# Performance work log

Hardware: AMD Instinct MI355X
Metric: run time of the kernel (lower is better)

## Reference

```python
import jax, jax.numpy as jnp
import numpy as np

DIM = 2048
N_HEADS = 32
N_KV_HEADS = 8
HEAD_DIM = DIM // N_HEADS  # 64
N_REP = N_HEADS // N_KV_HEADS  # 4
BSZ = 2
SEQ = 2048


def setup_inputs() -> dict:
    key = jax.random.key(0)
    ks = jax.random.split(key, 7)
    s = 0.02
    return {
        "x": jax.random.normal(ks[0], (BSZ, SEQ, DIM), dtype=jnp.float32),
        "freqs_cos": jnp.cos(jnp.outer(jnp.arange(SEQ, dtype=jnp.float32),
                                       1.0 / (10000.0 ** (jnp.arange(0, HEAD_DIM, 2, dtype=jnp.float32) / HEAD_DIM)))),
        "freqs_sin": jnp.sin(jnp.outer(jnp.arange(SEQ, dtype=jnp.float32),
                                       1.0 / (10000.0 ** (jnp.arange(0, HEAD_DIM, 2, dtype=jnp.float32) / HEAD_DIM)))),
        "wq": jax.random.normal(ks[1], (DIM, N_HEADS * HEAD_DIM), dtype=jnp.float32) * s,
        "wk": jax.random.normal(ks[2], (DIM, N_KV_HEADS * HEAD_DIM), dtype=jnp.float32) * s,
        "wv": jax.random.normal(ks[3], (DIM, N_KV_HEADS * HEAD_DIM), dtype=jnp.float32) * s,
        "wo": jax.random.normal(ks[4], (N_HEADS * HEAD_DIM, DIM), dtype=jnp.float32) * s,
    }


def _apply_rope(t, cos, sin):
    # t: [b, s, h, hd]; cos/sin: [s, hd/2] -> broadcast [1, s, 1, hd/2]
    tr = t.reshape(t.shape[:-1] + (HEAD_DIM // 2, 2))
    t_r, t_i = tr[..., 0], tr[..., 1]
    c = cos[None, :, None, :]
    s = sin[None, :, None, :]
    out_r = t_r * c - t_i * s
    out_i = t_r * s + t_i * c
    return jnp.stack([out_r, out_i], axis=-1).reshape(t.shape)


def reference(x, freqs_cos, freqs_sin, wq, wk, wv, wo):
    b, s, _ = x.shape
    xq = (x @ wq).reshape(b, s, N_HEADS, HEAD_DIM)
    xk = (x @ wk).reshape(b, s, N_KV_HEADS, HEAD_DIM)
    xv = (x @ wv).reshape(b, s, N_KV_HEADS, HEAD_DIM)

    xq = _apply_rope(xq, freqs_cos, freqs_sin)
    xk = _apply_rope(xk, freqs_cos, freqs_sin)

    # GQA: group query heads over kv heads instead of materializing repeated KV
    # xq -> [b, kv_heads, n_rep, s, hd]
    q = xq.transpose(0, 2, 1, 3).reshape(b, N_KV_HEADS, N_REP, s, HEAD_DIM)
    k = xk.transpose(0, 2, 1, 3)  # [b, kv, s, hd]
    v = xv.transpose(0, 2, 1, 3)  # [b, kv, s, hd]

    scale = 1.0 / jnp.sqrt(jnp.asarray(HEAD_DIM, dtype=x.dtype))
    scores = jnp.einsum("bgrqd,bgkd->bgrqk", q, k) * scale  # [b,kv,rep,s,s]
    causal = jnp.tril(jnp.ones((s, s), dtype=bool))
    scores = jnp.where(causal[None, None, None], scores, jnp.finfo(scores.dtype).min)
    probs = jax.nn.softmax(scores, axis=-1)
    out = jnp.einsum("bgrqk,bgkd->bgrqd", probs, v)  # [b,kv,rep,s,hd]
    out = out.reshape(b, N_HEADS, s, HEAD_DIM).transpose(0, 2, 1, 3).reshape(b, s, N_HEADS * HEAD_DIM)
    return out @ wo
```

## Files before the change

kernel.cpp:

```cpp
#include <hip/hip_runtime.h>

typedef unsigned short u16;
typedef unsigned int u32;
typedef __bf16 bf16x4 __attribute__((ext_vector_type(4)));
typedef __bf16 bf16x8 __attribute__((ext_vector_type(8)));
typedef float f32x4 __attribute__((ext_vector_type(4)));
typedef u32 u32x4 __attribute__((ext_vector_type(4)));

struct __align__(4) U16x2 { u16 x, y; };
struct __align__(8) U16x4 { u16 x, y, z, w; };

#define DEV static __device__ __forceinline__

extern "C" __device__ float __ocml_exp2_f32(float);
#if __has_builtin(__builtin_amdgcn_exp2f)
#define EXP2(x) __builtin_amdgcn_exp2f(x)
#else
#define EXP2(x) __ocml_exp2_f32(x)
#endif

DEV u16 f2bf(float f) {
  __bf16 h = (__bf16)f;
  return __builtin_bit_cast(u16, h);
}
DEV float bf2f(u16 u) { return __uint_as_float(((u32)u) << 16); }
DEV u32 pk2bf(float lo, float hi) { return (u32)f2bf(lo) | ((u32)f2bf(hi) << 16); }

DEV void gload16(const void* g, void* l) {
  __builtin_amdgcn_global_load_lds((const __attribute__((address_space(1))) char*)g,
                                   (__attribute__((address_space(3))) char*)l, 16, 0, 0);
}

DEV f32x4 mfma16(bf16x8 a, bf16x8 b, f32x4 c) {
  return __builtin_amdgcn_mfma_f32_16x16x32_bf16(a, b, c, 0, 0, 0);
}

__global__ __launch_bounds__(256) void cvt_x(const float* __restrict__ x, u16* __restrict__ xb) {
  int i = blockIdx.x * 256 + threadIdx.x;
  float4 v = ((const float4*)x)[i];
  U16x4 o;
  o.x = f2bf(v.x); o.y = f2bf(v.y); o.z = f2bf(v.z); o.w = f2bf(v.w);
  ((U16x4*)xb)[i] = o;
}

__global__ __launch_bounds__(256) void tconv(const float* __restrict__ src, u16* __restrict__ dst,
                                             int C, int nOff, int ldd) {
  __shared__ float t[32][33];
  int bx = blockIdx.x, by = blockIdx.y;
  int tx = threadIdx.x, ty = threadIdx.y;
#pragma unroll
  for (int j = 0; j < 4; ++j)
    t[ty + 8 * j][tx] = src[(size_t)(by * 32 + ty + 8 * j) * C + bx * 32 + tx];
  __syncthreads();
#pragma unroll
  for (int j = 0; j < 4; ++j)
    dst[(size_t)(nOff + bx * 32 + ty + 8 * j) * ldd + by * 32 + tx] = f2bf(t[tx][ty + 8 * j]);
}

__global__ __launch_bounds__(256) void vtrans(const u16* __restrict__ qkv, u16* __restrict__ Vt) {
  __shared__ u16 t[32][33];
  int bx = blockIdx.x, by = blockIdx.y, bz = blockIdx.z;
  int tx = threadIdx.x, ty = threadIdx.y;
  int b = bz >> 3, kh = bz & 7;
  const u16* src = qkv + (size_t)(b * 2048 + bx * 32) * 3072 + 2560 + kh * 64 + by * 32;
#pragma unroll
  for (int j = 0; j < 4; ++j) t[ty + 8 * j][tx] = src[(size_t)(ty + 8 * j) * 3072 + tx];
  __syncthreads();
  u16* dst = Vt + ((size_t)bz * 64 + by * 32) * 2048 + bx * 32;
#pragma unroll
  for (int j = 0; j < 4; ++j) dst[(size_t)(ty + 8 * j) * 2048 + tx] = t[tx][ty + 8 * j];
}

__global__ __launch_bounds__(256) void rope_qk(const u16* __restrict__ qkv,
                                               const float* __restrict__ fc,
                                               const float* __restrict__ fs,
                                               u16* __restrict__ Qo, u16* __restrict__ Ko) {
  int t = blockIdx.x * 256 + threadIdx.x;
  int d2 = t & 31;
  int rest = t >> 5;
  int h40 = rest % 40;
  int bs = rest / 40;
  int s = bs & 2047;
  int b = bs >> 11;
  const u16* src;
  u16* dst;
  float qscale;
  if (h40 < 32) {
    src = qkv + (size_t)bs * 3072 + h40 * 64 + 2 * d2;
    dst = Qo + (((size_t)(b * 32 + h40) * 2048 + s) * 64 + 2 * d2);
    qscale = 0.18033688011112042f;
  } else {
    int kh = h40 - 32;
    src = qkv + (size_t)bs * 3072 + 2048 + kh * 64 + 2 * d2;
    dst = Ko + (((size_t)(b * 8 + kh) * 2048 + s) * 64 + 2 * d2);
    qscale = 1.0f;
  }
  U16x2 v = *(const U16x2*)src;
  float xr = bf2f(v.x), xi = bf2f(v.y);
  float c = fc[s * 32 + d2] * qscale, sn = fs[s * 32 + d2] * qscale;
  U16x2 o;
  o.x = f2bf(xr * c - xi * sn);
  o.y = f2bf(xr * sn + xi * c);
  *(U16x2*)dst = o;
}

template <typename OutT>
__global__ __launch_bounds__(256, 2) void gemm_bt(const u16* __restrict__ A,
                                                  const u16* __restrict__ BT,
                                                  OutT* __restrict__ C,
                                                  int M, int N, int K) {
  __shared__ __align__(16) char smem[65536];
  const int tid = threadIdx.x;
  const int lane = tid & 63;
  const int wm = (tid >> 7) & 1, wn = (tid >> 6) & 1;
  const int tm = blockIdx.y, tn = blockIdx.x;
  const int Kb = K * 2;

  f32x4 acc[4][4];
#pragma unroll
  for (int i = 0; i < 4; ++i)
#pragma unroll
    for (int j = 0; j < 4; ++j) acc[i][j] = (f32x4){0.f, 0.f, 0.f, 0.f};

  const char* Ag = (const char*)A + (size_t)tm * 128 * Kb;
  const char* Bg = (const char*)BT + (size_t)tn * 128 * Kb;

  auto stage = [&](int buf, int t) {
#pragma unroll
    for (int i = 0; i < 4; ++i) {
      int vt = i * 256 + tid;
      int row = vt >> 3;
      int cb = (((vt & 7) << 4) ^ ((row & 7) << 4));
      gload16(Ag + (size_t)row * Kb + t * 128 + cb, smem + buf * 16384 + vt * 16);
      gload16(Bg + (size_t)row * Kb + t * 128 + cb, smem + 32768 + buf * 16384 + vt * 16);
    }
  };

  stage(0, 0);
  int cur = 0;
  const int NT = K >> 6;
  for (int t = 0; t < NT; ++t) {
    __syncthreads();
    if (t + 1 < NT) stage(cur ^ 1, t + 1);
    const char* As = smem + cur * 16384;
    const char* Bs = smem + 32768 + cur * 16384;
#pragma unroll
    for (int ks = 0; ks < 2; ++ks) {
      bf16x8 a[4], b[4];
#pragma unroll
      for (int mf = 0; mf < 4; ++mf) {
        int row = wm * 64 + mf * 16 + (lane & 15);
        int cb = (ks * 64 + ((lane >> 4) << 4)) ^ ((row & 7) << 4);
        a[mf] = *(const bf16x8*)(As + row * 128 + cb);
      }
#pragma unroll
      for (int nf = 0; nf < 4; ++nf) {
        int row = wn * 64 + nf * 16 + (lane & 15);
        int cb = (ks * 64 + ((lane >> 4) << 4)) ^ ((row & 7) << 4);
        b[nf] = *(const bf16x8*)(Bs + row * 128 + cb);
      }
#pragma unroll
      for (int mf = 0; mf < 4; ++mf)
#pragma unroll
        for (int nf = 0; nf < 4; ++nf) acc[mf][nf] = mfma16(a[mf], b[nf], acc[mf][nf]);
    }
    cur ^= 1;
  }
#pragma unroll
  for (int mf = 0; mf < 4; ++mf) {
    int row0 = tm * 128 + wm * 64 + mf * 16 + ((lane >> 4) << 2);
#pragma unroll
    for (int nf = 0; nf < 4; ++nf) {
      int col = tn * 128 + wn * 64 + nf * 16 + (lane & 15);
#pragma unroll
      for (int r = 0; r < 4; ++r) {
        float v = acc[mf][nf][r];
        if constexpr (sizeof(OutT) == 4)
          C[(size_t)(row0 + r) * N + col] = v;
        else
          C[(size_t)(row0 + r) * N + col] = f2bf(v);
      }
    }
  }
}

__global__ __launch_bounds__(128, 4) void attn(const u16* __restrict__ Q,
                                               const u16* __restrict__ Kt,
                                               const u16* __restrict__ Vt,
                                               u16* __restrict__ O) {
  __shared__ __align__(16) char smem[16384];

  const int tid = threadIdx.x, lane = tid & 63, w = tid >> 6;
  const int q15 = lane & 15, g = lane >> 4;
  const int bx = blockIdx.x, h = blockIdx.y, b = blockIdx.z;
  const int kh = h >> 2;
  const int QT0 = 63 - bx, QT1 = bx;

  const char* Qg = (const char*)(Q + ((size_t)(b * 32 + h) * 2048) * 64);
  const char* Kg = (const char*)(Kt + ((size_t)(b * 8 + kh) * 2048 * 64));
  const char* Vg = (const char*)(Vt + ((size_t)(b * 8 + kh) * 64 * 2048));

  bf16x8 qf0[2], qf1[2];
#pragma unroll
  for (int ks = 0; ks < 2; ++ks) {
    int r0 = QT0 * 32 + w * 16 + q15;
    int r1 = QT1 * 32 + w * 16 + q15;
    qf0[ks] = *(const bf16x8*)(Qg + (size_t)r0 * 128 + ks * 64 + (g << 4));
    qf1[ks] = *(const bf16x8*)(Qg + (size_t)r1 * 128 + ks * 64 + (g << 4));
  }

  f32x4 acc0[4], acc1[4];
#pragma unroll
  for (int j = 0; j < 4; ++j) {
    acc0[j] = (f32x4){0.f, 0.f, 0.f, 0.f};
    acc1[j] = (f32x4){0.f, 0.f, 0.f, 0.f};
  }
  float m0 = -1e30f, m1 = -1e30f, l0 = 0.f, l1 = 0.f;
  const f32x4 FZ = (f32x4){0.f, 0.f, 0.f, 0.f};

  auto stageKV = [&](int buf, int kt) {
#pragma unroll
    for (int i = 0; i < 2; ++i) {
      int vt = i * 128 + tid;
      int rho = vt >> 3, ck = vt & 7;
      int kap = ((rho & 12) << 1) + ((rho & 16) >> 2) + (rho & 3);
      gload16(Kg + (size_t)(kt * 32 + kap) * 128 + (((ck ^ rho) & 7) << 4),
              smem + buf * 8192 + vt * 16);
      int d = vt >> 2, cv = vt & 3;
      gload16(Vg + (size_t)d * 4096 + kt * 64 + (((cv ^ (d >> 1)) & 3) << 4),
              smem + buf * 8192 + 4096 + vt * 16);
    }
  };

  stageKV(0, 0);
  int cur = 0;
  const int nkt = QT0 + 1;
  for (int kt = 0; kt < nkt; ++kt) {
    __syncthreads();
    if (kt + 1 < nkt) stageKV(cur ^ 1, kt + 1);
    const char* Ks = smem + cur * 8192;
    const char* Vs = smem + cur * 8192 + 4096;
    const bool la = (kt <= QT1);

    bf16x8 kf[2][2];
#pragma unroll
    for (int ks = 0; ks < 2; ++ks)
#pragma unroll
      for (int nf = 0; nf < 2; ++nf) {
        int r = nf * 16 + q15;
        int c = (4 * ks + g) ^ (r & 7);
        kf[ks][nf] = *(const bf16x8*)(Ks + r * 128 + (c << 4));
      }

    f32x4 st0[2], st1[2];
    __builtin_amdgcn_s_setprio(1);
#pragma unroll
    for (int nf = 0; nf < 2; ++nf) {
      st0[nf] = mfma16(kf[0][nf], qf0[0], FZ);
      st0[nf] = mfma16(kf[1][nf], qf0[1], st0[nf]);
    }
    if (la) {
#pragma unroll
      for (int nf = 0; nf < 2; ++nf) {
        st1[nf] = mfma16(kf[0][nf], qf1[0], FZ);
        st1[nf] = mfma16(kf[1][nf], qf1[1], st1[nf]);
      }
    }
    __builtin_amdgcn_s_setprio(0);

    if (kt == QT0) {
      int qg = QT0 * 32 + w * 16 + q15;
#pragma unroll
      for (int nf = 0; nf < 2; ++nf)
#pragma unroll
        for (int r = 0; r < 4; ++r) {
          int kg = kt * 32 + 8 * g + 4 * nf + r;
          if (kg > qg) st0[nf][r] = -1e30f;
        }
    }
    if (la && kt == QT1) {
      int qg = QT1 * 32 + w * 16 + q15;
#pragma unroll
      for (int nf = 0; nf < 2; ++nf)
#pragma unroll
        for (int r = 0; r < 4; ++r) {
          int kg = kt * 32 + 8 * g + 4 * nf + r;
          if (kg > qg) st1[nf][r] = -1e30f;
        }
    }

    bf16x8 pa0, pa1;
#pragma unroll
    for (int t = 0; t < 2; ++t) {
      if (t == 1 && !la) break;
      f32x4* st = (t == 0) ? st0 : st1;
      float& m_r = (t == 0) ? m0 : m1;
      float& l_r = (t == 0) ? l0 : l1;
      f32x4* accT = (t == 0) ? acc0 : acc1;

      float vm = fmaxf(fmaxf(fmaxf(st[0][0], st[0][1]), fmaxf(st[0][2], st[0][3])),
                       fmaxf(fmaxf(st[1][0], st[1][1]), fmaxf(st[1][2], st[1][3])));
      vm = fmaxf(vm, __shfl_xor(vm, 16, 64));
      vm = fmaxf(vm, __shfl_xor(vm, 32, 64));
      const bool resc = !__all(vm - m_r <= 8.0f);
      if (resc) {
        float mn = fmaxf(m_r, vm);
        float cr = EXP2(m_r - mn);
        m_r = mn;
        l_r *= cr;
        float cra[4];
#pragma unroll
        for (int r = 0; r < 4; ++r) cra[r] = __shfl(cr, 4 * g + r, 64);
#pragma unroll
        for (int nfd = 0; nfd < 4; ++nfd)
#pragma unroll
          for (int r = 0; r < 4; ++r) accT[nfd][r] *= cra[r];
      }
      float vs = 0.f;
      u32x4 W;
      {
        float p0 = EXP2(st[0][0] - m_r), p1 = EXP2(st[0][1] - m_r);
        float p2 = EXP2(st[0][2] - m_r), p3 = EXP2(st[0][3] - m_r);
        float p4 = EXP2(st[1][0] - m_r), p5 = EXP2(st[1][1] - m_r);
        float p6 = EXP2(st[1][2] - m_r), p7 = EXP2(st[1][3] - m_r);
        vs = ((p0 + p1) + (p2 + p3)) + ((p4 + p5) + (p6 + p7));
        W.x = pk2bf(p0, p1);
        W.y = pk2bf(p2, p3);
        W.z = pk2bf(p4, p5);
        W.w = pk2bf(p6, p7);
      }
      if (t == 0) pa0 = __builtin_bit_cast(bf16x8, W);
      else pa1 = __builtin_bit_cast(bf16x8, W);
      vs += __shfl_xor(vs, 16, 64);
      vs += __shfl_xor(vs, 32, 64);
      l_r += vs;
    }

#pragma unroll
    for (int nfd = 0; nfd < 4; ++nfd) {
      int d = nfd * 16 + q15;
      int c = (g ^ (d >> 1)) & 3;
      bf16x8 vb = *(const bf16x8*)(Vs + d * 64 + (c << 4));
      __builtin_amdgcn_s_setprio(1);
      acc0[nfd] = mfma16(pa0, vb, acc0[nfd]);
      if (la) acc1[nfd] = mfma16(pa1, vb, acc1[nfd]);
      __builtin_amdgcn_s_setprio(0);
    }
    cur ^= 1;
  }

#pragma unroll
  for (int t = 0; t < 2; ++t) {
    float l_r = (t == 0) ? l0 : l1;
    f32x4* accT = (t == 0) ? acc0 : acc1;
    int qt = (t == 0) ? QT0 : QT1;
    u16* Og = O + ((size_t)(b * 2048 + qt * 32 + w * 16) * 2048 + h * 64);
    float la4[4];
#pragma unroll
    for (int r = 0; r < 4; ++r) la4[r] = __shfl(l_r, 4 * g + r, 64);
#pragma unroll
    for (int r = 0; r < 4; ++r) {
      float li = 1.f / la4[r];
#pragma unroll
      for (int nfd = 0; nfd < 4; ++nfd)
        Og[(size_t)(4 * g + r) * 2048 + nfd * 16 + q15] = f2bf(accT[nfd][r] * li);
    }
  }
}

extern "C" void kernel_launch(void* const* d_in, const int* in_sizes, int n_in,
                              void* d_out, int out_size, void* d_ws, size_t ws_size,
                              hipStream_t stream) {
  const float* x = (const float*)d_in[0];
  const float* fc = (const float*)d_in[1];
  const float* fs = (const float*)d_in[2];
  const float* wq = (const float*)d_in[3];
  const float* wk = (const float*)d_in[4];
  const float* wv = (const float*)d_in[5];
  const float* wo = (const float*)d_in[6];
  float* out = (float*)d_out;
  char* ws = (char*)d_ws;

  u16* xb    = (u16*)(ws);
  u16* qkv   = (u16*)(ws + 16777216);
  u16* woT   = (u16*)(ws + 41943040);
  u16* wqkvT = (u16*)(ws + 50331648);
  u16* Kbuf  = (u16*)(ws + 50331648);
  u16* Vtb   = (u16*)(ws + 54525952);
  u16* Qbuf = xb;
  u16* Obuf = qkv;

  dim3 tb(32, 8);
  cvt_x<<<dim3(8192), dim3(256), 0, stream>>>(x, xb);
  tconv<<<dim3(64, 64), tb, 0, stream>>>(wq, wqkvT, 2048, 0, 2048);
  tconv<<<dim3(16, 64), tb, 0, stream>>>(wk, wqkvT, 512, 2048, 2048);
  tconv<<<dim3(16, 64), tb, 0, stream>>>(wv, wqkvT, 512, 2560, 2048);
  tconv<<<dim3(64, 64), tb, 0, stream>>>(wo, woT, 2048, 0, 2048);
  gemm_bt<u16><<<dim3(24, 32), dim3(256), 0, stream>>>(xb, wqkvT, qkv, 4096, 3072, 2048);
  rope_qk<<<dim3(20480), dim3(256), 0, stream>>>(qkv, fc, fs, Qbuf, Kbuf);
  vtrans<<<dim3(64, 2, 16), tb, 0, stream>>>(qkv, Vtb);
  attn<<<dim3(32, 32, 2), dim3(128), 0, stream>>>(Qbuf, Kbuf, Vtb, Obuf);
  gemm_bt<float><<<dim3(16, 32), dim3(256), 0, stream>>>(Obuf, woT, out, 4096, 2048, 2048);
}
```

Before: 219.5 us.

## Fuse RoPE into QKV GEMM epilogue and restructure attention to 64-row query blocks

Applies RoPE and the query scale directly in the QKV GEMM epilogue, writing Q and K in head-major layout and V as a separate slice. This removes the rope_qk kernel and its extra pass over the qkv buffer. The attention kernel also changes from paired 32-row query tiles (balanced as 63-bx and bx) to a single 64-row block per 256-thread workgroup with 64-key tiles and a doubled LDS footprint. That drops the causal load-balancing pairing and the launch now runs longest blocks first. The epilogue also adds per-element shuffles and scattered frequency loads.

```diff
diff --git a/kernel.cpp b/kernel.cpp
--- a/kernel.cpp
+++ b/kernel.cpp
@@ -23,7 +23,6 @@
   __bf16 h = (__bf16)f;
   return __builtin_bit_cast(u16, h);
 }
-DEV float bf2f(u16 u) { return __uint_as_float(((u32)u) << 16); }
 DEV u32 pk2bf(float lo, float hi) { return (u32)f2bf(lo) | ((u32)f2bf(hi) << 16); }
 
 DEV void gload16(const void* g, void* l) {
@@ -57,64 +56,33 @@
     dst[(size_t)(nOff + bx * 32 + ty + 8 * j) * ldd + by * 32 + tx] = f2bf(t[tx][ty + 8 * j]);
 }
 
-__global__ __launch_bounds__(256) void vtrans(const u16* __restrict__ qkv, u16* __restrict__ Vt) {
+__global__ __launch_bounds__(256) void vtrans(const u16* __restrict__ Vsl, u16* __restrict__ Vt) {
   __shared__ u16 t[32][33];
   int bx = blockIdx.x, by = blockIdx.y, bz = blockIdx.z;
   int tx = threadIdx.x, ty = threadIdx.y;
   int b = bz >> 3, kh = bz & 7;
-  const u16* src = qkv + (size_t)(b * 2048 + bx * 32) * 3072 + 2560 + kh * 64 + by * 32;
-#pragma unroll
-  for (int j = 0; j < 4; ++j) t[ty + 8 * j][tx] = src[(size_t)(ty + 8 * j) * 3072 + tx];
+  const u16* src = Vsl + (size_t)(b * 2048 + bx * 32) * 512 + kh * 64 + by * 32;
+#pragma unroll
+  for (int j = 0; j < 4; ++j) t[ty + 8 * j][tx] = src[(size_t)(ty + 8 * j) * 512 + tx];
   __syncthreads();
   u16* dst = Vt + ((size_t)bz * 64 + by * 32) * 2048 + bx * 32;
 #pragma unroll
   for (int j = 0; j < 4; ++j) dst[(size_t)(ty + 8 * j) * 2048 + tx] = t[tx][ty + 8 * j];
 }
 
-__global__ __launch_bounds__(256) void rope_qk(const u16* __restrict__ qkv,
-                                               const float* __restrict__ fc,
-                                               const float* __restrict__ fs,
-                                               u16* __restrict__ Qo, u16* __restrict__ Ko) {
-  int t = blockIdx.x * 256 + threadIdx.x;
-  int d2 = t & 31;
-  int rest = t >> 5;
-  int h40 = rest % 40;
-  int bs = rest / 40;
-  int s = bs & 2047;
-  int b = bs >> 11;
-  const u16* src;
-  u16* dst;
-  float qscale;
-  if (h40 < 32) {
-    src = qkv + (size_t)bs * 3072 + h40 * 64 + 2 * d2;
-    dst = Qo + (((size_t)(b * 32 + h40) * 2048 + s) * 64 + 2 * d2);
-    qscale = 0.18033688011112042f;
-  } else {
-    int kh = h40 - 32;
-    src = qkv + (size_t)bs * 3072 + 2048 + kh * 64 + 2 * d2;
-    dst = Ko + (((size_t)(b * 8 + kh) * 2048 + s) * 64 + 2 * d2);
-    qscale = 1.0f;
-  }
-  U16x2 v = *(const U16x2*)src;
-  float xr = bf2f(v.x), xi = bf2f(v.y);
-  float c = fc[s * 32 + d2] * qscale, sn = fs[s * 32 + d2] * qscale;
-  U16x2 o;
-  o.x = f2bf(xr * c - xi * sn);
-  o.y = f2bf(xr * sn + xi * c);
-  *(U16x2*)dst = o;
-}
-
-template <typename OutT>
-__global__ __launch_bounds__(256, 2) void gemm_bt(const u16* __restrict__ A,
-                                                  const u16* __restrict__ BT,
-                                                  OutT* __restrict__ C,
-                                                  int M, int N, int K) {
+__global__ __launch_bounds__(256, 2) void gemm_qkv(const u16* __restrict__ A,
+                                                   const u16* __restrict__ BT,
+                                                   const float* __restrict__ fc,
+                                                   const float* __restrict__ fs,
+                                                   u16* __restrict__ Qo,
+                                                   u16* __restrict__ Ko,
+                                                   u16* __restrict__ Vsl) {
   __shared__ __align__(16) char smem[65536];
   const int tid = threadIdx.x;
   const int lane = tid & 63;
   const int wm = (tid >> 7) & 1, wn = (tid >> 6) & 1;
   const int tm = blockIdx.y, tn = blockIdx.x;
-  const int Kb = K * 2;
+  const int K = 2048, Kb = 4096, N = 3072;
 
   f32x4 acc[4][4];
 #pragma unroll
@@ -166,205 +134,299 @@
     }
     cur ^= 1;
   }
+
+  const float QS = 0.18033688011112042f;
 #pragma unroll
   for (int mf = 0; mf < 4; ++mf) {
     int row0 = tm * 128 + wm * 64 + mf * 16 + ((lane >> 4) << 2);
 #pragma unroll
     for (int nf = 0; nf < 4; ++nf) {
       int col = tn * 128 + wn * 64 + nf * 16 + (lane & 15);
-#pragma unroll
-      for (int r = 0; r < 4; ++r) {
-        float v = acc[mf][nf][r];
-        if constexpr (sizeof(OutT) == 4)
-          C[(size_t)(row0 + r) * N + col] = v;
-        else
-          C[(size_t)(row0 + r) * N + col] = f2bf(v);
-      }
-    }
-  }
-}
-
-__global__ __launch_bounds__(128, 4) void attn(const u16* __restrict__ Q,
+      if (col < 2560) {
+        int d = col & 63, d2 = d >> 1;
+        bool ev = !(col & 1);
+        bool isQ = (col < 2048);
+        int hh = isQ ? (col >> 6) : ((col - 2048) >> 6);
+#pragma unroll
+        for (int r = 0; r < 4; ++r) {
+          int row = row0 + r;
+          int bb = row >> 11, s = row & 2047;
+          float v = acc[mf][nf][r];
+          float p = __shfl_xor(v, 1, 64);
+          float c = fc[s * 32 + d2], sn = fs[s * 32 + d2];
+          if (isQ) { c *= QS; sn *= QS; }
+          float o = ev ? (v * c - p * sn) : (v * c + p * sn);
+          if (isQ)
+            Qo[((size_t)(bb * 32 + hh) * 2048 + s) * 64 + d] = f2bf(o);
+          else
+            Ko[((size_t)(bb * 8 + hh) * 2048 + s) * 64 + d] = f2bf(o);
+        }
+      } else {
+#pragma unroll
+        for (int r = 0; r < 4; ++r)
+          Vsl[(size_t)(row0 + r) * 512 + (col - 2560)] = f2bf(acc[mf][nf][r]);
+      }
+    }
+  }
+}
+
+__global__ __launch_bounds__(256, 2) void gemm_bt(const u16* __restrict__ A,
+                                                  const u16* __restrict__ BT,
+                                                  float* __restrict__ C,
+                                                  int M, int N, int K) {
+  __shared__ __align__(16) char smem[65536];
+  const int tid = threadIdx.x;
+  const int lane = tid & 63;
+  const int wm = (tid >> 7) & 1, wn = (tid >> 6) & 1;
+  const int tm = blockIdx.y, tn = blockIdx.x;
+  const int Kb = K * 2;
+
+  f32x4 acc[4][4];
+#pragma unroll
+  for (int i = 0; i < 4; ++i)
+#pragma unroll
+    for (int j = 0; j < 4; ++j) acc[i][j] = (f32x4){0.f, 0.f, 0.f, 0.f};
+
+  const char* Ag = (const char*)A + (size_t)tm * 128 * Kb;
+  const char* Bg = (const char*)BT + (size_t)tn * 128 * Kb;
+
+  auto stage = [&](int buf, int t) {
+#pragma unroll
+    for (int i = 0; i < 4; ++i) {
+      int vt = i * 256 + tid;
+      int row = vt >> 3;
+      int cb = (((vt & 7) << 4) ^ ((row & 7) << 4));
+      gload16(Ag + (size_t)row * Kb + t * 128 + cb, smem + buf * 16384 + vt * 16);
+      gload16(Bg + (size_t)row * Kb + t * 128 + cb, smem + 32768 + buf * 16384 + vt * 16);
+    }
+  };
+
+  stage(0, 0);
+  int cur = 0;
+  const int NT = K >> 6;
+  for (int t = 0; t < NT; ++t) {
+    __syncthreads();
+    if (t + 1 < NT) stage(cur ^ 1, t + 1);
+    const char* As = smem + cur * 16384;
+    const char* Bs = smem + 32768 + cur * 16384;
+#pragma unroll
+    for (int ks = 0; ks < 2; ++ks) {
+      bf16x8 a[4], b[4];
+#pragma unroll
+      for (int mf = 0; mf < 4; ++mf) {
+        int row = wm * 64 + mf * 16 + (lane & 15);
+        int cb = (ks * 64 + ((lane >> 4) << 4)) ^ ((row & 7) << 4);
+        a[mf] = *(const bf16x8*)(As + row * 128 + cb);
+      }
+#pragma unroll
+      for (int nf = 0; nf < 4; ++nf) {
+        int row = wn * 64 + nf * 16 + (lane & 15);
+        int cb = (ks * 64 + ((lane >> 4) << 4)) ^ ((row & 7) << 4);
+        b[nf] = *(const bf16x8*)(Bs + row * 128 + cb);
+      }
+#pragma unroll
+      for (int mf = 0; mf < 4; ++mf)
+#pragma unroll
+        for (int nf = 0; nf < 4; ++nf) acc[mf][nf] = mfma16(a[mf], b[nf], acc[mf][nf]);
+    }
+    cur ^= 1;
+  }
+#pragma unroll
+  for (int mf = 0; mf < 4; ++mf) {
+    int row0 = tm * 128 + wm * 64 + mf * 16 + ((lane >> 4) << 2);
+#pragma unroll
+    for (int nf = 0; nf < 4; ++nf) {
+      int col = tn * 128 + wn * 64 + nf * 16 + (lane & 15);
+#pragma unroll
+      for (int r = 0; r < 4; ++r)
+        C[(size_t)(row0 + r) * N + col] = acc[mf][nf][r];
+    }
+  }
+}
+
+__global__ __launch_bounds__(256, 4) void attn(const u16* __restrict__ Q,
                                                const u16* __restrict__ Kt,
                                                const u16* __restrict__ Vt,
                                                u16* __restrict__ O) {
-  __shared__ __align__(16) char smem[16384];
+  __shared__ __align__(16) char smem[32768];
 
   const int tid = threadIdx.x, lane = tid & 63, w = tid >> 6;
   const int q15 = lane & 15, g = lane >> 4;
-  const int bx = blockIdx.x, h = blockIdx.y, b = blockIdx.z;
+  const int qb = 31 - blockIdx.x;
+  const int h = blockIdx.y, b = blockIdx.z;
   const int kh = h >> 2;
-  const int QT0 = 63 - bx, QT1 = bx;
-
-  const char* Qg = (const char*)(Q + ((size_t)(b * 32 + h) * 2048) * 64);
+
+  const char* Qg = (const char*)(Q + (((size_t)(b * 32 + h) * 2048 + qb * 64) * 64));
   const char* Kg = (const char*)(Kt + ((size_t)(b * 8 + kh) * 2048 * 64));
   const char* Vg = (const char*)(Vt + ((size_t)(b * 8 + kh) * 64 * 2048));
 
-  bf16x8 qf0[2], qf1[2];
-#pragma unroll
-  for (int ks = 0; ks < 2; ++ks) {
-    int r0 = QT0 * 32 + w * 16 + q15;
-    int r1 = QT1 * 32 + w * 16 + q15;
-    qf0[ks] = *(const bf16x8*)(Qg + (size_t)r0 * 128 + ks * 64 + (g << 4));
-    qf1[ks] = *(const bf16x8*)(Qg + (size_t)r1 * 128 + ks * 64 + (g << 4));
-  }
-
-  f32x4 acc0[4], acc1[4];
-#pragma unroll
-  for (int j = 0; j < 4; ++j) {
-    acc0[j] = (f32x4){0.f, 0.f, 0.f, 0.f};
-    acc1[j] = (f32x4){0.f, 0.f, 0.f, 0.f};
-  }
-  float m0 = -1e30f, m1 = -1e30f, l0 = 0.f, l1 = 0.f;
+  bf16x8 qf[2];
+#pragma unroll
+  for (int ks = 0; ks < 2; ++ks)
+    qf[ks] = *(const bf16x8*)(Qg + (w * 16 + q15) * 128 + ks * 64 + (g << 4));
+
+  f32x4 acc[4];
+#pragma unroll
+  for (int j = 0; j < 4; ++j) acc[j] = (f32x4){0.f, 0.f, 0.f, 0.f};
+  float m_r = -1e30f, l_r = 0.f;
   const f32x4 FZ = (f32x4){0.f, 0.f, 0.f, 0.f};
 
   auto stageKV = [&](int buf, int kt) {
 #pragma unroll
     for (int i = 0; i < 2; ++i) {
-      int vt = i * 128 + tid;
+      int vt = i * 256 + tid;
       int rho = vt >> 3, ck = vt & 7;
-      int kap = ((rho & 12) << 1) + ((rho & 16) >> 2) + (rho & 3);
-      gload16(Kg + (size_t)(kt * 32 + kap) * 128 + (((ck ^ rho) & 7) << 4),
+      int kap = ((rho & 12) << 1) + ((rho & 16) >> 2) + (rho & 3) + ((rho >> 5) << 5);
+      gload16(Kg + (size_t)(kt * 64 + kap) * 128 + (((ck ^ rho) & 7) << 4),
               smem + buf * 8192 + vt * 16);
-      int d = vt >> 2, cv = vt & 3;
-      gload16(Vg + (size_t)d * 4096 + kt * 64 + (((cv ^ (d >> 1)) & 3) << 4),
-              smem + buf * 8192 + 4096 + vt * 16);
+      int d = vt >> 3, cv = vt & 7;
+      gload16(Vg + (size_t)d * 4096 + kt * 128 + (((cv ^ d) & 7) << 4),
+              smem + 16384 + buf * 8192 + vt * 16);
     }
   };
 
   stageKV(0, 0);
   int cur = 0;
-  const int nkt = QT0 + 1;
+  const int nkt = qb + 1;
   for (int kt = 0; kt < nkt; ++kt) {
     __syncthreads();
     if (kt + 1 < nkt) stageKV(cur ^ 1, kt + 1);
     const char* Ks = smem + cur * 8192;
-    const char* Vs = smem + cur * 8192 + 4096;
-    const bool la = (kt <= QT1);
-
-    bf16x8 kf[2][2];
-#pragma unroll
-    for (int ks = 0; ks < 2; ++ks)
-#pragma unroll
-      for (int nf = 0; nf < 2; ++nf) {
-        int r = nf * 16 + q15;
-        int c = (4 * ks + g) ^ (r & 7);
-        kf[ks][nf] = *(const bf16x8*)(Ks + r * 128 + (c << 4));
-      }
+    const char* Vs = smem + 16384 + cur * 8192;
+    const bool diag = (kt == qb);
+    const bool a1 = !(diag && w < 2);
 
     f32x4 st0[2], st1[2];
-    __builtin_amdgcn_s_setprio(1);
-#pragma unroll
-    for (int nf = 0; nf < 2; ++nf) {
-      st0[nf] = mfma16(kf[0][nf], qf0[0], FZ);
-      st0[nf] = mfma16(kf[1][nf], qf0[1], st0[nf]);
-    }
-    if (la) {
-#pragma unroll
-      for (int nf = 0; nf < 2; ++nf) {
-        st1[nf] = mfma16(kf[0][nf], qf1[0], FZ);
-        st1[nf] = mfma16(kf[1][nf], qf1[1], st1[nf]);
-      }
-    }
-    __builtin_amdgcn_s_setprio(0);
-
-    if (kt == QT0) {
-      int qg = QT0 * 32 + w * 16 + q15;
+    {
+      bf16x8 kf00, kf01, kf10, kf11;
+      kf00 = *(const bf16x8*)(Ks + (0 * 32 + 0 * 16 + q15) * 128 + (((0 + g) ^ (q15 & 7)) << 4));
+      kf01 = *(const bf16x8*)(Ks + (0 * 32 + 1 * 16 + q15) * 128 + (((0 + g) ^ (q15 & 7)) << 4));
+      bf16x8 kh00 = *(const bf16x8*)(Ks + (0 * 32 + 0 * 16 + q15) * 128 + (((4 + g) ^ (q15 & 7)) << 4));
+      bf16x8 kh01 = *(const bf16x8*)(Ks + (0 * 32 + 1 * 16 + q15) * 128 + (((4 + g) ^ (q15 & 7)) << 4));
+      __builtin_amdgcn_s_setprio(1);
+      st0[0] = mfma16(kf00, qf[0], FZ);
+      st0[1] = mfma16(kf01, qf[0], FZ);
+      st0[0] = mfma16(kh00, qf[1], st0[0]);
+      st0[1] = mfma16(kh01, qf[1], st0[1]);
+      __builtin_amdgcn_s_setprio(0);
+      if (a1) {
+        kf10 = *(const bf16x8*)(Ks + (32 + 0 * 16 + q15) * 128 + (((0 + g) ^ (q15 & 7)) << 4));
+        kf11 = *(const bf16x8*)(Ks + (32 + 1 * 16 + q15) * 128 + (((0 + g) ^ (q15 & 7)) << 4));
+        bf16x8 kh10 = *(const bf16x8*)(Ks + (32 + 0 * 16 + q15) * 128 + (((4 + g) ^ (q15 & 7)) << 4));
+        bf16x8 kh11 = *(const bf16x8*)(Ks + (32 + 1 * 16 + q15) * 128 + (((4 + g) ^ (q15 & 7)) << 4));
+        __builtin_amdgcn_s_setprio(1);
+        st1[0] = mfma16(kf10, qf[0], FZ);
+        st1[1] = mfma16(kf11, qf[0], FZ);
+        st1[0] = mfma16(kh10, qf[1], st1[0]);
+        st1[1] = mfma16(kh11, qf[1], st1[1]);
+        __builtin_amdgcn_s_setprio(0);
+      }
+    }
+
+    if (diag) {
+      int qg = qb * 64 + w * 16 + q15;
+      if (w < 2) {
+#pragma unroll
+        for (int nf = 0; nf < 2; ++nf)
+#pragma unroll
+          for (int r = 0; r < 4; ++r) {
+            int kg = kt * 64 + 8 * g + 4 * nf + r;
+            if (kg > qg) st0[nf][r] = -1e30f;
+          }
+      } else {
+#pragma unroll
+        for (int nf = 0; nf < 2; ++nf)
+#pragma unroll
+          for (int r = 0; r < 4; ++r) {
+            int kg = kt * 64 + 32 + 8 * g + 4 * nf + r;
+            if (kg > qg) st1[nf][r] = -1e30f;
+          }
+      }
+    }
+
+    float vm = st0[0][0];
+#pragma unroll
+    for (int nf = 0; nf < 2; ++nf)
+#pragma unroll
+      for (int r = 0; r < 4; ++r) vm = fmaxf(vm, st0[nf][r]);
+    if (a1) {
 #pragma unroll
       for (int nf = 0; nf < 2; ++nf)
 #pragma unroll
-        for (int r = 0; r < 4; ++r) {
-          int kg = kt * 32 + 8 * g + 4 * nf + r;
-          if (kg > qg) st0[nf][r] = -1e30f;
-        }
-    }
-    if (la && kt == QT1) {
-      int qg = QT1 * 32 + w * 16 + q15;
-#pragma unroll
-      for (int nf = 0; nf < 2; ++nf)
-#pragma unroll
-        for (int r = 0; r < 4; ++r) {
-          int kg = kt * 32 + 8 * g + 4 * nf + r;
-          if (kg > qg) st1[nf][r] = -1e30f;
-        }
-    }
-
+        for (int r = 0; r < 4; ++r) vm = fmaxf(vm, st1[nf][r]);
+    }
+    vm = fmaxf(vm, __shfl_xor(vm, 16, 64));
+    vm = fmaxf(vm, __shfl_xor(vm, 32, 64));
+    const bool resc = !__all(vm - m_r <= 8.0f);
+    if (resc) {
+      float mn = fmaxf(m_r, vm);
+      float cr = EXP2(m_r - mn);
+      m_r = mn;
+      l_r *= cr;
+      float cra[4];
+#pragma unroll
+      for (int r = 0; r < 4; ++r) cra[r] = __shfl(cr, 4 * g + r, 64);
+#pragma unroll
+      for (int nfd = 0; nfd < 4; ++nfd)
+#pragma unroll
+        for (int r = 0; r < 4; ++r) acc[nfd][r] *= cra[r];
+    }
+
+    float vs;
     bf16x8 pa0, pa1;
-#pragma unroll
-    for (int t = 0; t < 2; ++t) {
-      if (t == 1 && !la) break;
-      f32x4* st = (t == 0) ? st0 : st1;
-      float& m_r = (t == 0) ? m0 : m1;
-      float& l_r = (t == 0) ? l0 : l1;
-      f32x4* accT = (t == 0) ? acc0 : acc1;
-
-      float vm = fmaxf(fmaxf(fmaxf(st[0][0], st[0][1]), fmaxf(st[0][2], st[0][3])),
-                       fmaxf(fmaxf(st[1][0], st[1][1]), fmaxf(st[1][2], st[1][3])));
-      vm = fmaxf(vm, __shfl_xor(vm, 16, 64));
-      vm = fmaxf(vm, __shfl_xor(vm, 32, 64));
-      const bool resc = !__all(vm - m_r <= 8.0f);
-      if (resc) {
-        float mn = fmaxf(m_r, vm);
-        float cr = EXP2(m_r - mn);
-        m_r = mn;
-        l_r *= cr;
-        float cra[4];
-#pragma unroll
-        for (int r = 0; r < 4; ++r) cra[r] = __shfl(cr, 4 * g + r, 64);
-#pragma unroll
-        for (int nfd = 0; nfd < 4; ++nfd)
-#pragma unroll
-          for (int r = 0; r < 4; ++r) accT[nfd][r] *= cra[r];
-      }
-      float vs = 0.f;
+    {
+      float p0 = EXP2(st0[0][0] - m_r), p1 = EXP2(st0[0][1] - m_r);
+      float p2 = EXP2(st0[0][2] - m_r), p3 = EXP2(st0[0][3] - m_r);
+      float p4 = EXP2(st0[1][0] - m_r), p5 = EXP2(st0[1][1] - m_r);
+      float p6 = EXP2(st0[1][2] - m_r), p7 = EXP2(st0[1][3] - m_r);
+      vs = ((p0 + p1) + (p2 + p3)) + ((p4 + p5) + (p6 + p7));
       u32x4 W;
-      {
-        float p0 = EXP2(st[0][0] - m_r), p1 = EXP2(st[0][1] - m_r);
-        float p2 = EXP2(st[0][2] - m_r), p3 = EXP2(st[0][3] - m_r);
-        float p4 = EXP2(st[1][0] - m_r), p5 = EXP2(st[1][1] - m_r);
-        float p6 = EXP2(st[1][2] - m_r), p7 = EXP2(st[1][3] - m_r);
-        vs = ((p0 + p1) + (p2 + p3)) + ((p4 + p5) + (p6 + p7));
-        W.x = pk2bf(p0, p1);
-        W.y = pk2bf(p2, p3);
-        W.z = pk2bf(p4, p5);
-        W.w = pk2bf(p6, p7);
-      }
-      if (t == 0) pa0 = __builtin_bit_cast(bf16x8, W);
-      else pa1 = __builtin_bit_cast(bf16x8, W);
-      vs += __shfl_xor(vs, 16, 64);
-      vs += __shfl_xor(vs, 32, 64);
-      l_r += vs;
-    }
+      W.x = pk2bf(p0, p1); W.y = pk2bf(p2, p3);
+      W.z = pk2bf(p4, p5); W.w = pk2bf(p6, p7);
+      pa0 = __builtin_bit_cast(bf16x8, W);
+    }
+    if (a1) {
+      float p0 = EXP2(st1[0][0] - m_r), p1 = EXP2(st1[0][1] - m_r);
+      float p2 = EXP2(st1[0][2] - m_r), p3 = EXP2(st1[0][3] - m_r);
+      float p4 = EXP2(st1[1][0] - m_r), p5 = EXP2(st1[1][1] - m_r);
+      float p6 = EXP2(st1[1][2] - m_r), p7 = EXP2(st1[1][3] - m_r);
+      vs += ((p0 + p1) + (p2 + p3)) + ((p4 + p5) + (p6 + p7));
+      u32x4 W;
+      W.x = pk2bf(p0, p1); W.y = pk2bf(p2, p3);
+      W.z = pk2bf(p4, p5); W.w = pk2bf(p6, p7);
+      pa1 = __builtin_bit_cast(bf16x8, W);
+    }
+    vs += __shfl_xor(vs, 16, 64);
+    vs += __shfl_xor(vs, 32, 64);
+    l_r += vs;
 
 #pragma unroll
     for (int nfd = 0; nfd < 4; ++nfd) {
       int d = nfd * 16 + q15;
-      int c = (g ^ (d >> 1)) & 3;
-      bf16x8 vb = *(const bf16x8*)(Vs + d * 64 + (c << 4));
+      bf16x8 vb0 = *(const bf16x8*)(Vs + d * 128 + (((g ^ d) & 7) << 4));
       __builtin_amdgcn_s_setprio(1);
-      acc0[nfd] = mfma16(pa0, vb, acc0[nfd]);
-      if (la) acc1[nfd] = mfma16(pa1, vb, acc1[nfd]);
+      acc[nfd] = mfma16(pa0, vb0, acc[nfd]);
       __builtin_amdgcn_s_setprio(0);
+      if (a1) {
+        bf16x8 vb1 = *(const bf16x8*)(Vs + d * 128 + ((((4 + g) ^ d) & 7) << 4));
+        __builtin_amdgcn_s_setprio(1);
+        acc[nfd] = mfma16(pa1, vb1, acc[nfd]);
+        __builtin_amdgcn_s_setprio(0);
+      }
     }
     cur ^= 1;
   }
 
-#pragma unroll
-  for (int t = 0; t < 2; ++t) {
-    float l_r = (t == 0) ? l0 : l1;
-    f32x4* accT = (t == 0) ? acc0 : acc1;
-    int qt = (t == 0) ? QT0 : QT1;
-    u16* Og = O + ((size_t)(b * 2048 + qt * 32 + w * 16) * 2048 + h * 64);
-    float la4[4];
-#pragma unroll
-    for (int r = 0; r < 4; ++r) la4[r] = __shfl(l_r, 4 * g + r, 64);
-#pragma unroll
-    for (int r = 0; r < 4; ++r) {
-      float li = 1.f / la4[r];
-#pragma unroll
-      for (int nfd = 0; nfd < 4; ++nfd)
-        Og[(size_t)(4 * g + r) * 2048 + nfd * 16 + q15] = f2bf(accT[nfd][r] * li);
-    }
+  u16* Og = O + ((size_t)(b * 2048 + qb * 64 + w * 16) * 2048 + h * 64);
+  float la4[4];
+#pragma unroll
+  for (int r = 0; r < 4; ++r) la4[r] = __shfl(l_r, 4 * g + r, 64);
+#pragma unroll
+  for (int r = 0; r < 4; ++r) {
+    float li = 1.f / la4[r];
+#pragma unroll
+    for (int nfd = 0; nfd < 4; ++nfd)
+      Og[(size_t)(4 * g + r) * 2048 + nfd * 16 + q15] = f2bf(acc[nfd][r] * li);
   }
 }
 
@@ -382,13 +444,13 @@
   char* ws = (char*)d_ws;
 
   u16* xb    = (u16*)(ws);
-  u16* qkv   = (u16*)(ws + 16777216);
-  u16* woT   = (u16*)(ws + 41943040);
-  u16* wqkvT = (u16*)(ws + 50331648);
-  u16* Kbuf  = (u16*)(ws + 50331648);
-  u16* Vtb   = (u16*)(ws + 54525952);
-  u16* Qbuf = xb;
-  u16* Obuf = qkv;
+  u16* Qb    = (u16*)(ws + 16777216);
+  u16* Kb    = (u16*)(ws + 33554432);
+  u16* Vsl   = (u16*)(ws + 37748736);
+  u16* Vtb   = (u16*)(ws + 41943040);
+  u16* woT   = (u16*)(ws + 46137344);
+  u16* wqkvT = (u16*)(ws + 54525952);
+  u16* Obuf = xb;
 
   dim3 tb(32, 8);
   cvt_x<<<dim3(8192), dim3(256), 0, stream>>>(x, xb);
@@ -396,9 +458,8 @@
   tconv<<<dim3(16, 64), tb, 0, stream>>>(wk, wqkvT, 512, 2048, 2048);
   tconv<<<dim3(16, 64), tb, 0, stream>>>(wv, wqkvT, 512, 2560, 2048);
   tconv<<<dim3(64, 64), tb, 0, stream>>>(wo, woT, 2048, 0, 2048);
-  gemm_bt<u16><<<dim3(24, 32), dim3(256), 0, stream>>>(xb, wqkvT, qkv, 4096, 3072, 2048);
-  rope_qk<<<dim3(20480), dim3(256), 0, stream>>>(qkv, fc, fs, Qbuf, Kbuf);
-  vtrans<<<dim3(64, 2, 16), tb, 0, stream>>>(qkv, Vtb);
-  attn<<<dim3(32, 32, 2), dim3(128), 0, stream>>>(Qbuf, Kbuf, Vtb, Obuf);
-  gemm_bt<float><<<dim3(16, 32), dim3(256), 0, stream>>>(Obuf, woT, out, 4096, 2048, 2048);
-}
+  gemm_qkv<<<dim3(24, 32), dim3(256), 0, stream>>>(xb, wqkvT, fc, fs, Qb, Kb, Vsl);
+  vtrans<<<dim3(64, 2, 16), tb, 0, stream>>>(Vsl, Vtb);
+  attn<<<dim3(32, 32, 2), dim3(256), 0, stream>>>(Qb, Kb, Vtb, Obuf);
+  gemm_bt<<<dim3(16, 32), dim3(256), 0, stream>>>(Obuf, woT, out, 4096, 2048, 2048);
+}
```

New measurement: 236.1 us. +7.6%, slower.
